# Kernel optimization log

Measured on AMD Instinct MI355X. Metric: run time of the kernel, lower is better.

Reference implementation:

```python
import jax, jax.numpy as jnp
import numpy as np

EPS = 1e-5
DIM = 32          # head_dim
HEADS = 8         # in_channels // dim * heads_ratio = 256 // 32

def hardswish(x):
    return x * jnp.clip(x + 3.0, 0.0, 6.0) / 6.0

def conv1x1(x, w):
    # w: (C_out, C_in); x: (B, C_in, H, W)
    return jnp.einsum('oi,bihw->bohw', w, x)

def dwconv(x, w, pad):
    # depthwise conv, w: (C, 1, kh, kw)
    return jax.lax.conv_general_dilated(
        x, w, (1, 1), [(pad, pad), (pad, pad)],
        dimension_numbers=('NCHW', 'OIHW', 'NCHW'),
        feature_group_count=x.shape[1])

def gconv1x1(x, w, groups):
    # grouped 1x1 conv, w: (C_out, C_in//groups, 1, 1)
    return jax.lax.conv_general_dilated(
        x, w, (1, 1), [(0, 0), (0, 0)],
        dimension_numbers=('NCHW', 'OIHW', 'NCHW'),
        feature_group_count=groups)


def setup_inputs() -> dict:
    key = jax.random.key(0)
    ks = jax.random.split(key, 12)
    B, C, H, W = 16, 256, 32, 32
    td = HEADS * DIM          # 256 (total_dim per branch)
    c3 = 3 * td               # 768
    mid = 4 * C               # 1024 (expand_ratio=4)

    def rn(k, shape, fan_in):
        return jax.random.normal(k, shape, jnp.float32) * (1.0 / np.sqrt(fan_in))

    return {
        'x': jax.random.normal(ks[0], (B, C, H, W), jnp.float32),
        # LiteMLA
        'w_qkv': rn(ks[1], (c3, C), C),                 # 1x1, bias=False, no norm
        'w_agg_dw': rn(ks[2], (c3, 1, 5, 5), 25),       # depthwise 5x5, pad 2
        'w_agg_pw': rn(ks[3], (c3, DIM, 1, 1), DIM),    # grouped 1x1, groups=3*HEADS
        'w_proj': rn(ks[4], (C, 2 * td), 2 * td),       # 1x1, bias=False (BN follows)
        'bn_proj_scale': jnp.ones((C,), jnp.float32) + 0.1 * jax.random.normal(ks[5], (C,), jnp.float32),
        'bn_proj_bias': 0.1 * jax.random.normal(ks[6], (C,), jnp.float32),
        # MBConv
        'w_mb1': rn(ks[7], (mid, C), C),
        'b_mb1': jnp.zeros((mid,), jnp.float32),
        'w_mb_dw': rn(ks[8], (mid, 1, 3, 3), 9),
        'b_mb_dw': jnp.zeros((mid,), jnp.float32),
        'w_mb2': rn(ks[9], (C, mid), mid),              # bias=False (BN follows)
        'bn2_scale': jnp.ones((C,), jnp.float32) + 0.1 * jax.random.normal(ks[10], (C,), jnp.float32),
        'bn2_bias': 0.1 * jax.random.normal(ks[11], (C,), jnp.float32),
    }


def reference(x, w_qkv, w_agg_dw, w_agg_pw, w_proj, bn_proj_scale, bn_proj_bias,
              w_mb1, b_mb1, w_mb_dw, b_mb_dw, w_mb2, bn2_scale, bn2_bias):
    B, C, H, W = x.shape
    # ---- LiteMLA context module (residual) ----
    qkv = conv1x1(x, w_qkv)                                   # (B, 768, H, W)
    agg = gconv1x1(dwconv(qkv, w_agg_dw, 2), w_agg_pw, 3 * HEADS)
    ms = jnp.concatenate([qkv, agg], axis=1)                  # (B, 1536, H, W)
    nh = ms.shape[1] // (3 * DIM)                             # 16 total heads
    t = ms.reshape(B, nh, 3 * DIM, H * W).transpose(0, 1, 3, 2)  # (B, nh, HW, 3*DIM)
    q, k, v = jnp.split(t, 3, axis=-1)                        # each (B, nh, HW, DIM)
    q = jax.nn.relu(q).astype(jnp.float32)
    k = jax.nn.relu(k).astype(jnp.float32)
    v = jnp.pad(v.astype(jnp.float32), ((0, 0), (0, 0), (0, 0), (0, 1)),
                constant_values=1.0)                          # (B, nh, HW, DIM+1)
    kv = jnp.einsum('bhnd,bhne->bhde', k, v)                  # (B, nh, DIM, DIM+1)
    out = jnp.einsum('bhnd,bhde->bhne', q, kv)                # (B, nh, HW, DIM+1)
    out = out[..., :-1] / (out[..., -1:] + EPS)
    out = out.astype(x.dtype)
    out = out.transpose(0, 1, 3, 2).reshape(B, nh * DIM, H, W)  # (B, 512, H, W)
    out = conv1x1(out, w_proj)
    out = out * bn_proj_scale[:, None, None] + bn_proj_bias[:, None, None]
    x = x + out                                               # residual
    # ---- MBConv local module (residual) ----
    h = hardswish(conv1x1(x, w_mb1) + b_mb1[:, None, None])
    h = hardswish(dwconv(h, w_mb_dw, 1) + b_mb_dw[:, None, None])
    h = conv1x1(h, w_mb2)
    h = h * bn2_scale[:, None, None] + bn2_bias[:, None, None]
    return x + h
```

## Files before the change

kernel.cpp:

```cpp
#include <hip/hip_runtime.h>
#include <hip/hip_bf16.h>


typedef unsigned short u16;
typedef __attribute__((ext_vector_type(8))) short short8;
typedef __attribute__((ext_vector_type(4))) short short4v;
typedef __attribute__((ext_vector_type(4))) float f32x4;

#define HW 1024
#define EPSV 1e-5f
#define MFMA16(a, b, c) __builtin_amdgcn_mfma_f32_16x16x32_bf16((a), (b), (c), 0, 0, 0)
#define FB(n) ((((n) ^ ((n) >> 3))) & 7)

__device__ __forceinline__ u16 f2bf(float f) {
    union { __hip_bfloat16 h; u16 u; } c; c.h = __float2bfloat16(f); return c.u;
}
__device__ __forceinline__ float bf2f(u16 u) {
    union { u16 u; __hip_bfloat16 h; } c; c.u = u; return __bfloat162float(c.h);
}
__device__ __forceinline__ float hswish(float v) {
    return v * fminf(fmaxf(v + 3.f, 0.f), 6.f) * (1.f / 6.f);
}
__device__ __forceinline__ void gload_lds16(const u16* g, u16* lds) {
    __builtin_amdgcn_global_load_lds(
        (const __attribute__((address_space(1))) void*)g,
        (__attribute__((address_space(3))) void*)lds, 16, 0, 0);
}

__global__ __launch_bounds__(256) void prep_k(
    const float* __restrict__ x,  u16* __restrict__ xb,
    const float* __restrict__ wq, u16* __restrict__ wqb,
    const float* __restrict__ wp, u16* __restrict__ wpb,
    const float* __restrict__ w1, u16* __restrict__ w1b,
    const float* __restrict__ w2, u16* __restrict__ w2b)
{
    const int N0 = 4194304, N1 = 196608, N2 = 131072, N3 = 262144;
    const int total = N0 + N1 + N2 + N3 + 262144;
    for (int i = blockIdx.x * 256 + threadIdx.x; i < total; i += gridDim.x * 256) {
        int id = i;
        if (id < N0) { xb[id]  = f2bf(x[id]);  continue; } id -= N0;
        if (id < N1) { wqb[id] = f2bf(wq[id]); continue; } id -= N1;
        if (id < N2) { wpb[id] = f2bf(wp[id]); continue; } id -= N2;
        if (id < N3) { w1b[id] = f2bf(w1[id]); continue; } id -= N3;
        w2b[id] = f2bf(w2[id]);
    }
}

template<int EPI, int TM>
__global__ __launch_bounds__(TM * 2) void gemm_bf(
    const u16* __restrict__ A, const u16* __restrict__ Bact,
    const float* __restrict__ s1, const float* __restrict__ s2,
    const float* __restrict__ Rres, float* __restrict__ outF,
    u16* __restrict__ outB, int M, int K)
{
    constexpr int NW = TM / 32;
    constexpr int NT = TM * 2;
    const int b  = blockIdx.z;
    const int n0 = blockIdx.x * 128;
    const int m0 = blockIdx.y * TM;
    const int t  = threadIdx.x;
    const int l  = t & 63, w = t >> 6;
    const int lr = t & 15, lg = (t >> 4) & 3;
    const int wm = (TM == 128) ? (w >> 1) : 0;
    const int wn = (TM == 128) ? (w & 1) : w;

    __shared__ __attribute__((aligned(16))) u16 As[TM * 64];
    __shared__ __attribute__((aligned(16))) u16 Bs[128 * 64];

    const u16* Ab0 = A + (size_t)m0 * K;
    const u16* Bp  = Bact + (size_t)b * K * HW + n0;

    int brow[4], bfb[4];
    #pragma unroll
    for (int j = 0; j < 4; ++j) {
        brow[j] = wn * 64 + j * 16 + lr;
        bfb[j]  = FB(brow[j]);
    }

    f32x4 zero4 = {0.f, 0.f, 0.f, 0.f};
    f32x4 acc[4][4];
    #pragma unroll
    for (int i = 0; i < 4; ++i)
        #pragma unroll
        for (int j = 0; j < 4; ++j) acc[i][j] = zero4;

    for (int k0 = 0; k0 < K; k0 += 64) {
        #pragma unroll
        for (int u = 0; u < 4; ++u) {
            int g = (u * NW + w) * 64 + l;
            int row = g >> 3, cl = g & 7;
            int cs = cl ^ (row & 7);
            gload_lds16(Ab0 + (size_t)row * K + k0 + cs * 8,
                        As + (size_t)(u * NW + w) * 512);
        }
        #pragma unroll
        for (int q = 0; q < 256 / NT; ++q) {
            const int kc = (t >> 5) + q * (NT / 32);
            const int n4 = t & 31;
            short4v v[8];
            #pragma unroll
            for (int kk = 0; kk < 8; ++kk)
                v[kk] = *(const short4v*)(Bp + (size_t)(k0 + kc * 8 + kk) * HW + n4 * 4);
            #pragma unroll
            for (int nn = 0; nn < 4; ++nn) {
                const int n = n4 * 4 + nn;
                short8 wv = { v[0][nn], v[1][nn], v[2][nn], v[3][nn],
                              v[4][nn], v[5][nn], v[6][nn], v[7][nn] };
                *(short8*)(&Bs[n * 64 + ((kc ^ FB(n)) * 8)]) = wv;
            }
        }
        __syncthreads();
        #pragma unroll
        for (int kk = 0; kk < 2; ++kk) {
            short8 a[4], bb[4];
            #pragma unroll
            for (int i = 0; i < 4; ++i) {
                int row = wm * 64 + i * 16 + lr;
                a[i] = *(const short8*)(&As[row * 64 + (((kk * 4 + lg) ^ (lr & 7)) * 8)]);
            }
            #pragma unroll
            for (int j = 0; j < 4; ++j)
                bb[j] = *(const short8*)(&Bs[brow[j] * 64 + (((kk * 4 + lg) ^ bfb[j]) * 8)]);
            #pragma unroll
            for (int i = 0; i < 4; ++i)
                #pragma unroll
                for (int j = 0; j < 4; ++j)
                    acc[i][j] = MFMA16(a[i], bb[j], acc[i][j]);
        }
        __syncthreads();
    }

    const size_t obase = (size_t)b * M * HW;
    #pragma unroll
    for (int i = 0; i < 4; ++i) {
        #pragma unroll
        for (int r = 0; r < 4; ++r) {
            const int grow = m0 + wm * 64 + i * 16 + lg * 4 + r;
            float p1 = 0.f, p2 = 0.f;
            if (EPI == 1) { p1 = s1[grow]; }
            if (EPI >= 2) { p1 = s1[grow]; p2 = s2[grow]; }
            #pragma unroll
            for (int j = 0; j < 4; ++j) {
                const int gcol = n0 + wn * 64 + j * 16 + lr;
                const size_t off = obase + (size_t)grow * HW + gcol;
                float v = acc[i][j][r];
                if (EPI == 0) { outB[off] = f2bf(v); }
                if (EPI == 1) { v = hswish(v + p1); outB[off] = f2bf(v); }
                if (EPI == 2) { v = v * p1 + p2 + Rres[off]; outF[off] = v; outB[off] = f2bf(v); }
                if (EPI == 3) { v = v * p1 + p2 + Rres[off]; outF[off] = v; }
            }
        }
    }
}

template<int KS, int PAD, int NCH, bool HS>
__global__ __launch_bounds__(256) void dwconv_k(
    const u16* __restrict__ in, const float* __restrict__ w,
    const float* __restrict__ bias, u16* __restrict__ out)
{
    constexpr int T = 32 + 2 * PAD;
    __shared__ float tile[T * T];
    const int plane = blockIdx.x;
    const int c = plane % NCH;
    const u16* ip = in + (size_t)plane * HW;
    const int t = threadIdx.x;
    for (int idx = t; idx < T * T; idx += 256) {
        int r = idx / T, cc = idx % T;
        int gr = r - PAD, gc = cc - PAD;
        float v = 0.f;
        if ((unsigned)gr < 32u && (unsigned)gc < 32u) v = bf2f(ip[gr * 32 + gc]);
        tile[idx] = v;
    }
    float wl[KS * KS];
    #pragma unroll
    for (int u = 0; u < KS * KS; ++u) wl[u] = w[c * KS * KS + u];
    const float bv = HS ? bias[c] : 0.f;
    __syncthreads();
    #pragma unroll
    for (int pj = 0; pj < 4; ++pj) {
        const int px = t + pj * 256;
        const int pr = px >> 5, pc = px & 31;
        float s = bv;
        #pragma unroll
        for (int dr = 0; dr < KS; ++dr)
            #pragma unroll
            for (int dc = 0; dc < KS; ++dc)
                s += tile[(pr + dr) * T + pc + dc] * wl[dr * KS + dc];
        if (HS) s = hswish(s);
        out[(size_t)plane * HW + px] = f2bf(s);
    }
}

__global__ __launch_bounds__(256) void gconv_k(
    const u16* __restrict__ dw, const float* __restrict__ wpw,
    u16* __restrict__ agg)
{
    const int gx = blockIdx.x;
    const int g = gx >> 2, nt = gx & 3;
    const int b = blockIdx.y;
    const int n0 = nt * 256;
    const int t = threadIdx.x;
    __shared__ float dt[32][256];
    __shared__ float wl[32 * 32];
    const u16* dp = dw + ((size_t)b * 768 + g * 32) * HW + n0;
    for (int idx = t; idx < 32 * 256; idx += 256) {
        int i = idx >> 8, nn = idx & 255;
        dt[i][nn] = bf2f(dp[(size_t)i * HW + nn]);
    }
    for (int idx = t; idx < 1024; idx += 256) wl[idx] = wpw[g * 1024 + idx];
    __syncthreads();
    float acc[32] = {};
    #pragma unroll
    for (int i = 0; i < 32; ++i) {
        const float d = dt[i][t];
        #pragma unroll
        for (int oc = 0; oc < 32; ++oc) acc[oc] += wl[oc * 32 + i] * d;
    }
    u16* ap = agg + ((size_t)b * 768 + g * 32) * HW + n0;
    #pragma unroll
    for (int oc = 0; oc < 32; ++oc) ap[(size_t)oc * HW + t] = f2bf(acc[oc]);
}

__global__ __launch_bounds__(64) void kv_k(
    const u16* __restrict__ qkvb, const u16* __restrict__ aggb,
    float* __restrict__ kvp)
{
    const int blk = blockIdx.x;
    const int bh = blk >> 2, nc = blk & 3;
    const int b = bh >> 4, h = bh & 15;
    const u16* src = (h < 8) ? qkvb + ((size_t)b * 768 + h * 96) * HW
                             : aggb + ((size_t)b * 768 + (h - 8) * 96) * HW;
    const u16* kp = src + 32 * HW + nc * 256;
    const u16* vp = src + 64 * HW + nc * 256;
    const int l = threadIdx.x;
    const int lr = l & 15, lg = l >> 4;

    f32x4 zero4 = {0.f, 0.f, 0.f, 0.f};
    f32x4 acc[2][3];
    #pragma unroll
    for (int i = 0; i < 2; ++i)
        #pragma unroll
        for (int j = 0; j < 3; ++j) acc[i][j] = zero4;

    short8 bones;
    #pragma unroll
    for (int g = 0; g < 8; ++g) bones[g] = (lr == 0) ? (short)0x3F80 : (short)0;

    for (int ks = 0; ks < 8; ++ks) {
        const int kn = ks * 32 + lg * 8;
        short8 a0 = *(const short8*)(kp + (size_t)lr * HW + kn);
        short8 a1 = *(const short8*)(kp + (size_t)(16 + lr) * HW + kn);
        #pragma unroll
        for (int g = 0; g < 8; ++g) {
            if (((u16)a0[g]) & 0x8000) a0[g] = 0;
            if (((u16)a1[g]) & 0x8000) a1[g] = 0;
        }
        short8 b0 = *(const short8*)(vp + (size_t)lr * HW + kn);
        short8 b1 = *(const short8*)(vp + (size_t)(16 + lr) * HW + kn);
        acc[0][0] = MFMA16(a0, b0, acc[0][0]);
        acc[0][1] = MFMA16(a0, b1, acc[0][1]);
        acc[0][2] = MFMA16(a0, bones, acc[0][2]);
        acc[1][0] = MFMA16(a1, b0, acc[1][0]);
        acc[1][1] = MFMA16(a1, b1, acc[1][1]);
        acc[1][2] = MFMA16(a1, bones, acc[1][2]);
    }
    float* dst = kvp + (size_t)blk * 1056;
    #pragma unroll
    for (int dt = 0; dt < 2; ++dt)
        #pragma unroll
        for (int et = 0; et < 3; ++et)
            #pragma unroll
            for (int r = 0; r < 4; ++r) {
                const int d = dt * 16 + lg * 4 + r;
                const int e = et * 16 + lr;
                if (et < 2 || lr == 0) dst[d * 33 + e] = acc[dt][et][r];
            }
}

__global__ __launch_bounds__(256) void attn_k(
    const u16* __restrict__ qkvb, const u16* __restrict__ aggb,
    const float* __restrict__ kvp, u16* __restrict__ attnb)
{
    const int blk = blockIdx.x;
    const int bh = blk >> 2, nc = blk & 3;
    const int b = bh >> 4, h = bh & 15;
    const u16* qp = (h < 8) ? qkvb + ((size_t)b * 768 + h * 96) * HW
                            : aggb + ((size_t)b * 768 + (h - 8) * 96) * HW;
    __shared__ u16 qs[256 * 40];
    const int t = threadIdx.x;
    #pragma unroll 4
    for (int u = 0; u < 32; ++u) {
        int id = t + u * 256;
        int d = id >> 8, n = id & 255;
        u16 q = qp[(size_t)d * HW + nc * 256 + n];
        if (q & 0x8000) q = 0;
        qs[n * 40 + d] = q;
    }
    const int lr = t & 15, lg = (t >> 4) & 3, w = t >> 6;

    short8 bf[3];
    const float* kb = kvp + (size_t)bh * 4 * 1056;
    #pragma unroll
    for (int et = 0; et < 3; ++et)
        #pragma unroll
        for (int j = 0; j < 8; ++j) {
            const int d = lg * 8 + j, e = et * 16 + lr;
            float s = 0.f;
            if (e <= 32) {
                #pragma unroll
                for (int c = 0; c < 4; ++c) s += kb[c * 1056 + d * 33 + e];
            }
            bf[et][j] = (short)f2bf(s);
        }
    __syncthreads();

    f32x4 zero4 = {0.f, 0.f, 0.f, 0.f};
    f32x4 acc[4][3];
    #pragma unroll
    for (int i = 0; i < 4; ++i) {
        const int row = w * 64 + i * 16 + lr;
        short8 a = *(const short8*)(&qs[row * 40 + lg * 8]);
        #pragma unroll
        for (int et = 0; et < 3; ++et) acc[i][et] = MFMA16(a, bf[et], zero4);
    }

    u16* ap = attnb + (size_t)b * 512 * HW + (size_t)h * 32 * HW;
    #pragma unroll
    for (int i = 0; i < 4; ++i) {
        float inv[4];
        #pragma unroll
        for (int r = 0; r < 4; ++r) {
            const float den = __shfl(acc[i][2][r], t & 48, 64);
            inv[r] = 1.f / (den + EPSV);
        }
        const int nbase = nc * 256 + w * 64 + i * 16 + lg * 4;
        #pragma unroll
        for (int et = 0; et < 2; ++et) {
            const int e = et * 16 + lr;
            short4v o;
            #pragma unroll
            for (int r = 0; r < 4; ++r) o[r] = (short)f2bf(acc[i][et][r] * inv[r]);
            *(short4v*)(ap + (size_t)e * HW + nbase) = o;
        }
    }
}

extern "C" void kernel_launch(void* const* d_in, const int* in_sizes, int n_in,
                              void* d_out, int out_size, void* d_ws, size_t ws_size,
                              hipStream_t stream)
{
    const float* x        = (const float*)d_in[0];
    const float* w_qkv    = (const float*)d_in[1];
    const float* w_agg_dw = (const float*)d_in[2];
    const float* w_agg_pw = (const float*)d_in[3];
    const float* w_proj   = (const float*)d_in[4];
    const float* bnp_s    = (const float*)d_in[5];
    const float* bnp_b    = (const float*)d_in[6];
    const float* w_mb1    = (const float*)d_in[7];
    const float* b_mb1    = (const float*)d_in[8];
    const float* w_mb_dw  = (const float*)d_in[9];
    const float* b_mb_dw  = (const float*)d_in[10];
    const float* w_mb2    = (const float*)d_in[11];
    const float* bn2_s    = (const float*)d_in[12];
    const float* bn2_b    = (const float*)d_in[13];
    float* out = (float*)d_out;
    char*  W   = (char*)d_ws;

    u16*   qkvb  = (u16*)(W + 0);
    u16*   xb    = (u16*)(W + 25165824);
    u16*   dwb   = (u16*)(W + 33554432);
    u16*   aggb  = (u16*)(W + 58720256);
    float* kvp   = (float*)(W + 83886080);
    u16*   attnb = (u16*)(W + 33554432);
    u16*   h1b   = (u16*)(W + 0);
    u16*   h2b   = (u16*)(W + 58720256);
    float* y1f   = (float*)(W + 92274688);
    u16*   y1b   = (u16*)(W + 109051904);
    u16*   wqb   = (u16*)(W + 117440512);
    u16*   wpb   = (u16*)(W + 117833728);
    u16*   w1b   = (u16*)(W + 118095872);
    u16*   w2b   = (u16*)(W + 118620160);

    prep_k<<<2048, 256, 0, stream>>>(x, xb, w_qkv, wqb, w_proj, wpb,
                                     w_mb1, w1b, w_mb2, w2b);
    gemm_bf<0, 128><<<dim3(8, 6, 16), 256, 0, stream>>>(
        wqb, xb, nullptr, nullptr, nullptr, nullptr, qkvb, 768, 256);
    dwconv_k<5, 2, 768, false><<<dim3(16 * 768), 256, 0, stream>>>(
        qkvb, w_agg_dw, nullptr, dwb);
    gconv_k<<<dim3(96, 16), 256, 0, stream>>>(dwb, w_agg_pw, aggb);
    kv_k<<<dim3(1024), 64, 0, stream>>>(qkvb, aggb, kvp);
    attn_k<<<dim3(1024), 256, 0, stream>>>(qkvb, aggb, kvp, attnb);
    gemm_bf<2, 64><<<dim3(8, 4, 16), 128, 0, stream>>>(
        wpb, attnb, bnp_s, bnp_b, x, y1f, y1b, 256, 512);
    gemm_bf<1, 128><<<dim3(8, 8, 16), 256, 0, stream>>>(
        w1b, y1b, b_mb1, nullptr, nullptr, nullptr, h1b, 1024, 256);
    dwconv_k<3, 1, 1024, true><<<dim3(16 * 1024), 256, 0, stream>>>(
        h1b, w_mb_dw, b_mb_dw, h2b);
    gemm_bf<3, 64><<<dim3(8, 4, 16), 128, 0, stream>>>(
        w2b, h2b, bn2_s, bn2_b, y1f, out, nullptr, 256, 1024);
}
```

Baseline: 268.9 us.

## Double-buffer GEMM LDS tiles and prefetch next K tile during MFMA

Converts the bf16 GEMM main loop to a double-buffered scheme. A for the next tile is issued straight to LDS and B is read into registers before the MFMA work on the current tile, then B is written to the alternate buffer afterwards. This drops one barrier per iteration and overlaps global-load latency with compute. The cost is twice the LDS use and extra registers holding the B tile, which may lower occupancy.

```diff
diff --git a/kernel.cpp b/kernel.cpp
--- a/kernel.cpp
+++ b/kernel.cpp
@@ -55,6 +55,9 @@
 {
     constexpr int NW = TM / 32;
     constexpr int NT = TM * 2;
+    constexpr int NQ = 256 / NT;
+    constexpr int ABUF = TM * 64;
+    constexpr int BBUF = 128 * 64;
     const int b  = blockIdx.z;
     const int n0 = blockIdx.x * 128;
     const int m0 = blockIdx.y * TM;
@@ -64,8 +67,8 @@
     const int wm = (TM == 128) ? (w >> 1) : 0;
     const int wn = (TM == 128) ? (w & 1) : w;
 
-    __shared__ __attribute__((aligned(16))) u16 As[TM * 64];
-    __shared__ __attribute__((aligned(16))) u16 Bs[128 * 64];
+    __shared__ __attribute__((aligned(16))) u16 As[2 * ABUF];
+    __shared__ __attribute__((aligned(16))) u16 Bs[2 * BBUF];
 
     const u16* Ab0 = A + (size_t)m0 * K;
     const u16* Bp  = Bact + (size_t)b * K * HW + n0;
@@ -77,57 +80,87 @@
         bfb[j]  = FB(brow[j]);
     }
 
-    f32x4 zero4 = {0.f, 0.f, 0.f, 0.f};
-    f32x4 acc[4][4];
-    #pragma unroll
-    for (int i = 0; i < 4; ++i)
-        #pragma unroll
-        for (int j = 0; j < 4; ++j) acc[i][j] = zero4;
-
-    for (int k0 = 0; k0 < K; k0 += 64) {
+    short4v breg[NQ][8];
+
+    auto issueA = [&](int k0, int sel) {
+        u16* dst = As + (size_t)sel * ABUF;
         #pragma unroll
         for (int u = 0; u < 4; ++u) {
             int g = (u * NW + w) * 64 + l;
             int row = g >> 3, cl = g & 7;
             int cs = cl ^ (row & 7);
             gload_lds16(Ab0 + (size_t)row * K + k0 + cs * 8,
-                        As + (size_t)(u * NW + w) * 512);
-        }
-        #pragma unroll
-        for (int q = 0; q < 256 / NT; ++q) {
+                        dst + (size_t)(u * NW + w) * 512);
+        }
+    };
+    auto loadB = [&](int k0) {
+        #pragma unroll
+        for (int q = 0; q < NQ; ++q) {
             const int kc = (t >> 5) + q * (NT / 32);
             const int n4 = t & 31;
-            short4v v[8];
             #pragma unroll
             for (int kk = 0; kk < 8; ++kk)
-                v[kk] = *(const short4v*)(Bp + (size_t)(k0 + kc * 8 + kk) * HW + n4 * 4);
+                breg[q][kk] = *(const short4v*)(Bp + (size_t)(k0 + kc * 8 + kk) * HW + n4 * 4);
+        }
+    };
+    auto writeB = [&](int sel) {
+        u16* dst = Bs + (size_t)sel * BBUF;
+        #pragma unroll
+        for (int q = 0; q < NQ; ++q) {
+            const int kc = (t >> 5) + q * (NT / 32);
+            const int n4 = t & 31;
             #pragma unroll
             for (int nn = 0; nn < 4; ++nn) {
                 const int n = n4 * 4 + nn;
-                short8 wv = { v[0][nn], v[1][nn], v[2][nn], v[3][nn],
-                              v[4][nn], v[5][nn], v[6][nn], v[7][nn] };
-                *(short8*)(&Bs[n * 64 + ((kc ^ FB(n)) * 8)]) = wv;
+                short8 wv = { breg[q][0][nn], breg[q][1][nn], breg[q][2][nn],
+                              breg[q][3][nn], breg[q][4][nn], breg[q][5][nn],
+                              breg[q][6][nn], breg[q][7][nn] };
+                *(short8*)(&dst[n * 64 + ((kc ^ FB(n)) * 8)]) = wv;
             }
         }
-        __syncthreads();
+    };
+
+    f32x4 zero4 = {0.f, 0.f, 0.f, 0.f};
+    f32x4 acc[4][4];
+    #pragma unroll
+    for (int i = 0; i < 4; ++i)
+        #pragma unroll
+        for (int j = 0; j < 4; ++j) acc[i][j] = zero4;
+
+    const int ntk = K >> 6;
+    issueA(0, 0);
+    loadB(0);
+    writeB(0);
+    __syncthreads();
+
+    int cur = 0;
+    for (int tile = 0; tile < ntk; ++tile) {
+        const int nxt = cur ^ 1;
+        const bool pf = (tile + 1 < ntk);
+        if (pf) { issueA((tile + 1) << 6, nxt); loadB((tile + 1) << 6); }
+
+        const u16* Asb = As + (size_t)cur * ABUF;
+        const u16* Bsb = Bs + (size_t)cur * BBUF;
         #pragma unroll
         for (int kk = 0; kk < 2; ++kk) {
             short8 a[4], bb[4];
             #pragma unroll
             for (int i = 0; i < 4; ++i) {
                 int row = wm * 64 + i * 16 + lr;
-                a[i] = *(const short8*)(&As[row * 64 + (((kk * 4 + lg) ^ (lr & 7)) * 8)]);
+                a[i] = *(const short8*)(&Asb[row * 64 + (((kk * 4 + lg) ^ (lr & 7)) * 8)]);
             }
             #pragma unroll
             for (int j = 0; j < 4; ++j)
-                bb[j] = *(const short8*)(&Bs[brow[j] * 64 + (((kk * 4 + lg) ^ bfb[j]) * 8)]);
+                bb[j] = *(const short8*)(&Bsb[brow[j] * 64 + (((kk * 4 + lg) ^ bfb[j]) * 8)]);
             #pragma unroll
             for (int i = 0; i < 4; ++i)
                 #pragma unroll
                 for (int j = 0; j < 4; ++j)
                     acc[i][j] = MFMA16(a[i], bb[j], acc[i][j]);
         }
+        if (pf) writeB(nxt);
         __syncthreads();
+        cur = nxt;
     }
 
     const size_t obase = (size_t)b * M * HW;
```

Result: no change. 266.3 us (-1.0%).
